# Kernel optimization log

Hardware: AMD Instinct MI355X
Metric: run time of the kernel (lower is better)

Reference implementation:

```python
import jax, jax.numpy as jnp
import numpy as np
from jax import lax

B, C, H, W = 16, 128, 128, 128
COUT, KH, KW, K, RED, TEMP = 128, 3, 3, 4, 4, 30.0
ATTN_CH = max(C // RED, 1)

def setup_inputs() -> dict:
    key = jax.random.key(0)
    ks = jax.random.split(key, 7)
    fan_out = COUT * KH * KW
    std = np.sqrt(2.0 / fan_out)  # kaiming_normal fan_out, relu
    return {
        "x": jax.random.normal(ks[0], (B, C, H, W), dtype=jnp.float32),
        "weight": jax.random.normal(ks[1], (K, COUT, C, KH, KW), dtype=jnp.float32) * std,
        "bias": jnp.zeros((K, COUT), dtype=jnp.float32),
        "aw1": jax.random.normal(ks[2], (ATTN_CH, C), dtype=jnp.float32) * (1.0 / np.sqrt(C)),
        "ab1": jnp.zeros((ATTN_CH,), dtype=jnp.float32),
        "aw2": jax.random.normal(ks[3], (K, ATTN_CH), dtype=jnp.float32) * (1.0 / np.sqrt(ATTN_CH)),
        "ab2": jnp.zeros((K,), dtype=jnp.float32),
    }

def reference(x, weight, bias, aw1, ab1, aw2, ab2):
    # Attention branch: global avg pool -> 1x1 conv -> relu -> 1x1 conv
    pooled = jnp.mean(x, axis=(2, 3))                       # (B, C)
    h = jax.nn.relu(pooled @ aw1.T + ab1)                   # (B, attn_ch)
    scores = h @ aw2.T + ab2                                # (B, K)
    attn = jax.nn.softmax(scores / TEMP, axis=1)            # (B, K)

    # Per-sample aggregated kernel and bias
    agg_w = jnp.einsum('bk,koipq->boipq', attn, weight)     # (B, Cout, Cin, kH, kW)
    agg_b = attn @ bias                                     # (B, Cout)

    # Per-sample conv2d (stride 1, padding 1, dilation 1, groups 1)
    def conv_one(xi, wi):
        return lax.conv_general_dilated(
            xi[None], wi,
            window_strides=(1, 1),
            padding=((1, 1), (1, 1)),
            dimension_numbers=('NCHW', 'OIHW', 'NCHW'),
        )[0]

    out = jax.vmap(conv_one)(x, agg_w)                      # (B, Cout, H, W)
    return out + agg_b[:, :, None, None]
```

## Files before the change

### kernel.cpp

```cpp
#include <hip/hip_runtime.h>

typedef float f32x4 __attribute__((ext_vector_type(4)));
typedef short bf16x8 __attribute__((ext_vector_type(8)));

__device__ __forceinline__ unsigned short f2bf(float f) {
  unsigned u = __builtin_bit_cast(unsigned, f);
  u = (u + 0x7FFFu + ((u >> 16) & 1u)) >> 16;
  return (unsigned short)u;
}

__device__ __forceinline__ void async16(const unsigned short* g, unsigned short* l) {
  __builtin_amdgcn_global_load_lds(
      (__attribute__((address_space(1))) void*)g,
      (__attribute__((address_space(3))) void*)l, 16, 0, 0);
}

#define XT_ROW 16640

__global__ __launch_bounds__(256) void k_transpose(const float* __restrict__ x,
                                                   unsigned short* __restrict__ xt,
                                                   float* __restrict__ rowsum) {
  __shared__ unsigned short tile[128][128];
  __shared__ float psum[128][8];
  const int y = blockIdx.x, b = blockIdx.y;
  const int t = threadIdx.x;
  const int colb = (t & 7) * 16;
  const int cp = t >> 3;
  const int swz = (t & 7) << 3;
  for (int ci = 0; ci < 4; ++ci) {
    const int c = ci * 32 + cp;
    const int c2 = c ^ swz;
    const float* src = x + (((size_t)(b * 128 + c) * 128 + y) * 128 + colb);
    float s = 0.f;
#pragma unroll
    for (int j = 0; j < 16; j += 4) {
      float4 v = *(const float4*)(src + j);
      s += v.x + v.y + v.z + v.w;
      tile[colb + j + 0][c2] = f2bf(v.x);
      tile[colb + j + 1][c2] = f2bf(v.y);
      tile[colb + j + 2][c2] = f2bf(v.z);
      tile[colb + j + 3][c2] = f2bf(v.w);
    }
    psum[c][t & 7] = s;
  }
  __syncthreads();
#pragma unroll
  for (int it = 0; it < 8; ++it) {
    const int slot = t + it * 256;
    const int col = slot >> 4;
    const int cg = (slot & 15) * 8;
    const int c2 = cg ^ (((col >> 4) & 7) << 3);
    uint4 vv = *(const uint4*)&tile[col][c2];
    *(uint4*)(xt + (((size_t)b * 130 + y + 1) * 130 + col + 1) * 128 + cg) = vv;
  }
  if (t < 128) {
    float r = 0.f;
#pragma unroll
    for (int j = 0; j < 8; ++j) r += psum[t][j];
    rowsum[((size_t)b * 128 + t) * 128 + y] = r;
  }
}

__global__ __launch_bounds__(256) void k_border(unsigned short* __restrict__ xt) {
  const int b = blockIdx.y;
  const int idx = blockIdx.x * 256 + threadIdx.x;
  if (idx >= 8256) return;
  int row, col, ck;
  if (idx < 4160) {
    row = (idx < 2080) ? 0 : 129;
    const int s = idx % 2080;
    col = s >> 4;
    ck = s & 15;
  } else {
    const int s = idx - 4160;
    row = (s >> 5) + 1;
    col = (s & 16) ? 129 : 0;
    ck = s & 15;
  }
  uint4 z = {0, 0, 0, 0};
  *(uint4*)(xt + ((size_t)b * 130 + row) * 130 * 128 + (size_t)col * 128 + ck * 8) = z;
}

__global__ __launch_bounds__(128) void k_attn(const float* __restrict__ rowsum,
                                              const float* __restrict__ aw1,
                                              const float* __restrict__ ab1,
                                              const float* __restrict__ aw2,
                                              const float* __restrict__ ab2,
                                              const float* __restrict__ bias,
                                              float* __restrict__ attn,
                                              float* __restrict__ aggb) {
  __shared__ float pooled[128];
  __shared__ float h[32];
  __shared__ float at[4];
  const int b = blockIdx.x, t = threadIdx.x;
  const float* rs = rowsum + (size_t)(b * 128 + t) * 128;
  float s = 0.f;
  for (int yy = 0; yy < 128; ++yy) s += rs[yy];
  pooled[t] = s * (1.f / 16384.f);
  __syncthreads();
  if (t < 32) {
    float hv = ab1[t];
    for (int c = 0; c < 128; ++c) hv += pooled[c] * aw1[t * 128 + c];
    h[t] = fmaxf(hv, 0.f);
  }
  __syncthreads();
  if (t < 4) {
    float sc = ab2[t];
    for (int a = 0; a < 32; ++a) sc += h[a] * aw2[t * 32 + a];
    at[t] = sc * (1.f / 30.f);
  }
  __syncthreads();
  if (t == 0) {
    float m = fmaxf(fmaxf(at[0], at[1]), fmaxf(at[2], at[3]));
    float e0 = __expf(at[0] - m), e1 = __expf(at[1] - m);
    float e2 = __expf(at[2] - m), e3 = __expf(at[3] - m);
    float inv = 1.f / (e0 + e1 + e2 + e3);
    at[0] = e0 * inv; at[1] = e1 * inv; at[2] = e2 * inv; at[3] = e3 * inv;
  }
  __syncthreads();
  if (t < 4) attn[b * 4 + t] = at[t];
  float ab = 0.f;
  for (int k = 0; k < 4; ++k) ab += at[k] * bias[k * 128 + t];
  aggb[b * 128 + t] = ab;
}

__global__ __launch_bounds__(256) void k_aggw(const float* __restrict__ weight,
                                              const float* __restrict__ attn,
                                              unsigned short* __restrict__ aggw) {
  const int fid = blockIdx.x * 256 + threadIdx.x;
  const int kk = fid & 63;
  const int o = (fid >> 6) & 127;
  const int rest = fid >> 13;
  const int s = rest % 18;
  const int b = rest / 18;
  const int c = ((s & 1) << 6) + kk;
  const int pq = s >> 1;
  const size_t src = (size_t)o * 1152 + (size_t)c * 9 + pq;
  float v = attn[b * 4 + 0] * weight[src]
          + attn[b * 4 + 1] * weight[src + 147456]
          + attn[b * 4 + 2] * weight[src + 2 * 147456]
          + attn[b * 4 + 3] * weight[src + 3 * 147456];
  aggw[fid] = f2bf(v);
}

__global__ __launch_bounds__(512, 2) void k_conv(const unsigned short* __restrict__ xt,
                                                 const unsigned short* __restrict__ aggw,
                                                 const float* __restrict__ aggb,
                                                 float* __restrict__ out) {
  __shared__ unsigned short lds[3][24576];
  const int id = blockIdx.x;
  const int swz = (id & 7) * 128 + (id >> 3);
  const int b = swz >> 6;
  const int y0 = (swz & 63) * 2;
  const int t = threadIdx.x;
  const int lane = t & 63, w = t >> 6;
  const int mw = w >> 2, nw = w & 3;
  const int l15 = lane & 15, lk = lane >> 4;
  const int rswz = (l15 & 7) * 8;

  const unsigned short* aS[2];
  int aD[2];
#pragma unroll
  for (int i = 0; i < 2; ++i) {
    const int ca = w * 128 + i * 64 + lane;
    const int n = ca >> 3, k8 = ca & 7;
    aS[i] = aggw + (size_t)b * 147456 + n * 64 + ((k8 ^ (n & 7)) * 8);
    aD[i] = w * 1024 + i * 512;
  }
  const unsigned short* bS[4];
  int bD[4];
#pragma unroll
  for (int i = 0; i < 4; ++i) {
    const int cb = w * 256 + i * 64 + lane;
    const int r = cb >> 10, n = (cb >> 3) & 127, k8 = cb & 7;
    bS[i] = xt + ((size_t)(b * 130 + y0 + r) * 130 + n) * 128 + ((k8 ^ (n & 7)) * 8);
    bD[i] = 8192 + w * 2048 + i * 512;
  }

#define STAGE(buf, s) {                                                        \
    const int tap_ = (s) >> 1, c0_ = ((s) & 1) << 6;                           \
    const int p_ = tap_ / 3, q_ = tap_ - 3 * p_;                               \
    _Pragma("unroll")                                                          \
    for (int i = 0; i < 2; ++i)                                                \
      async16(aS[i] + (s) * 8192, &lds[buf][0] + aD[i]);                       \
    _Pragma("unroll")                                                          \
    for (int i = 0; i < 4; ++i)                                                \
      async16(bS[i] + p_ * XT_ROW + q_ * 128 + c0_, &lds[buf][0] + bD[i]);     \
  }

  f32x4 acc[4][4] = {};
  STAGE(0, 0);
  STAGE(1, 1);

#pragma unroll
  for (int s = 0; s < 18; ++s) {
    const int cur = s % 3;
    if (s < 17) { asm volatile("s_waitcnt vmcnt(6)" ::: "memory"); }
    else       { asm volatile("s_waitcnt vmcnt(0)" ::: "memory"); }
    __builtin_amdgcn_sched_barrier(0);
    __builtin_amdgcn_s_barrier();
    __builtin_amdgcn_sched_barrier(0);
    if (s + 2 < 18) STAGE((s + 2) % 3, s + 2);
    __builtin_amdgcn_sched_barrier(0);

    const unsigned short* A0 = &lds[cur][0];
    const unsigned short* B0 = &lds[cur][8192];
#pragma unroll
    for (int kk = 0; kk < 2; ++kk) {
      bf16x8 af[4], bfr[4];
#pragma unroll
      for (int mi = 0; mi < 4; ++mi)
        af[mi] = *(const bf16x8*)(A0 + (mw * 64 + mi * 16 + l15) * 64
                                     + ((kk * 32 + lk * 8) ^ rswz));
#pragma unroll
      for (int ni = 0; ni < 4; ++ni)
        bfr[ni] = *(const bf16x8*)(B0 + (nw * 64 + ni * 16 + l15) * 64
                                      + ((kk * 32 + lk * 8) ^ rswz));
      __builtin_amdgcn_s_setprio(1);
#pragma unroll
      for (int mi = 0; mi < 4; ++mi)
#pragma unroll
        for (int ni = 0; ni < 4; ++ni)
          acc[mi][ni] = __builtin_amdgcn_mfma_f32_16x16x32_bf16(af[mi], bfr[ni], acc[mi][ni], 0, 0, 0);
      __builtin_amdgcn_s_setprio(0);
    }
  }
#undef STAGE

  const int r_ = nw >> 1;
  const int y = y0 + r_;
  const int colb = (nw & 1) * 64 + l15;
#pragma unroll
  for (int mi = 0; mi < 4; ++mi) {
    const int o = mw * 64 + mi * 16 + lk * 4;
#pragma unroll
    for (int rr = 0; rr < 4; ++rr) {
      const float bsv = aggb[b * 128 + o + rr];
      float* orow = out + ((size_t)(b * 128 + o + rr) * 128 + y) * 128 + colb;
      orow[0]  = acc[mi][0][rr] + bsv;
      orow[16] = acc[mi][1][rr] + bsv;
      orow[32] = acc[mi][2][rr] + bsv;
      orow[48] = acc[mi][3][rr] + bsv;
    }
  }
}

extern "C" void kernel_launch(void* const* d_in, const int* in_sizes, int n_in,
                              void* d_out, int out_size, void* d_ws, size_t ws_size,
                              hipStream_t stream) {
  const float* x      = (const float*)d_in[0];
  const float* weight = (const float*)d_in[1];
  const float* bias   = (const float*)d_in[2];
  const float* aw1    = (const float*)d_in[3];
  const float* ab1    = (const float*)d_in[4];
  const float* aw2    = (const float*)d_in[5];
  const float* ab2    = (const float*)d_in[6];
  float* out = (float*)d_out;

  char* ws = (char*)d_ws;
  unsigned short* xt   = (unsigned short*)ws;
  unsigned short* aggw = (unsigned short*)(ws + 69222400);
  float* rowsum        = (float*)(ws + 69222400 + 4718592);
  float* attn          = (float*)(ws + 69222400 + 4718592 + 1048576);
  float* aggb          = (float*)(ws + 69222400 + 4718592 + 1048576 + 256);

  hipLaunchKernelGGL(k_border, dim3(33, 16), dim3(256), 0, stream, xt);
  hipLaunchKernelGGL(k_transpose, dim3(128, 16), dim3(256), 0, stream, x, xt, rowsum);
  hipLaunchKernelGGL(k_attn, dim3(16), dim3(128), 0, stream,
                     rowsum, aw1, ab1, aw2, ab2, bias, attn, aggb);
  hipLaunchKernelGGL(k_aggw, dim3(9216), dim3(256), 0, stream, weight, attn, aggw);
  hipLaunchKernelGGL(k_conv, dim3(1024), dim3(512), 0, stream, xt, aggw, aggb, out);
}
```

Baseline: 158.3 us.

## Shrink conv tile to one output row with 32-channel K slices and 3 blocks/CU

The conv kernel now computes one output row (128 out channels x 128 pixels) per 256-thread block instead of two rows per 512-thread block. The K dimension is split into 36 stages of 32 channels instead of 18 stages of 64, so LDS use per block drops threefold and occupancy rises to 3 blocks per CU. The aggregated-weight layout and the LDS swizzle are changed to match the 32-wide chunks. The aim is more concurrent blocks to hide latency, at the cost of twice as many barriers per unit of work and less reuse of the weight tile across rows.

```diff
diff --git a/kernel.cpp b/kernel.cpp
--- a/kernel.cpp
+++ b/kernel.cpp
@@ -128,13 +128,13 @@
                                               const float* __restrict__ attn,
                                               unsigned short* __restrict__ aggw) {
   const int fid = blockIdx.x * 256 + threadIdx.x;
-  const int kk = fid & 63;
-  const int o = (fid >> 6) & 127;
-  const int rest = fid >> 13;
-  const int s = rest % 18;
-  const int b = rest / 18;
-  const int c = ((s & 1) << 6) + kk;
-  const int pq = s >> 1;
+  const int kk = fid & 31;
+  const int o = (fid >> 5) & 127;
+  const int rest = fid >> 12;
+  const int s = rest % 36;
+  const int b = rest / 36;
+  const int c = ((s & 3) << 5) + kk;
+  const int pq = s >> 2;
   const size_t src = (size_t)o * 1152 + (size_t)c * 9 + pq;
   float v = attn[b * 4 + 0] * weight[src]
           + attn[b * 4 + 1] * weight[src + 147456]
@@ -143,49 +143,41 @@
   aggw[fid] = f2bf(v);
 }
 
-__global__ __launch_bounds__(512, 2) void k_conv(const unsigned short* __restrict__ xt,
+__global__ __launch_bounds__(256, 3) void k_conv(const unsigned short* __restrict__ xt,
                                                  const unsigned short* __restrict__ aggw,
                                                  const float* __restrict__ aggb,
                                                  float* __restrict__ out) {
-  __shared__ unsigned short lds[3][24576];
+  __shared__ unsigned short lds[3][8192];
   const int id = blockIdx.x;
-  const int swz = (id & 7) * 128 + (id >> 3);
-  const int b = swz >> 6;
-  const int y0 = (swz & 63) * 2;
+  const int swz = (id & 7) * 256 + (id >> 3);
+  const int b = swz >> 7, y = swz & 127;
   const int t = threadIdx.x;
   const int lane = t & 63, w = t >> 6;
-  const int mw = w >> 2, nw = w & 3;
+  const int mw = w >> 1, nw = w & 1;
   const int l15 = lane & 15, lk = lane >> 4;
-  const int rswz = (l15 & 7) * 8;
+  const int rswz = (l15 & 3) * 8;
 
   const unsigned short* aS[2];
-  int aD[2];
+  const unsigned short* bS[2];
+  int dA[2], dB[2];
 #pragma unroll
   for (int i = 0; i < 2; ++i) {
-    const int ca = w * 128 + i * 64 + lane;
-    const int n = ca >> 3, k8 = ca & 7;
-    aS[i] = aggw + (size_t)b * 147456 + n * 64 + ((k8 ^ (n & 7)) * 8);
-    aD[i] = w * 1024 + i * 512;
-  }
-  const unsigned short* bS[4];
-  int bD[4];
-#pragma unroll
-  for (int i = 0; i < 4; ++i) {
-    const int cb = w * 256 + i * 64 + lane;
-    const int r = cb >> 10, n = (cb >> 3) & 127, k8 = cb & 7;
-    bS[i] = xt + ((size_t)(b * 130 + y0 + r) * 130 + n) * 128 + ((k8 ^ (n & 7)) * 8);
-    bD[i] = 8192 + w * 2048 + i * 512;
+    const int c = i * 256 + t;
+    const int n = c >> 2, k8 = c & 3;
+    const int sk = (k8 ^ (n & 3)) * 8;
+    aS[i] = aggw + (size_t)b * 147456 + n * 32 + sk;
+    bS[i] = xt + ((size_t)(b * 130 + y) * 130 + n) * 128 + sk;
+    dA[i] = i * 2048 + w * 512;
+    dB[i] = 4096 + i * 2048 + w * 512;
   }
 
 #define STAGE(buf, s) {                                                        \
-    const int tap_ = (s) >> 1, c0_ = ((s) & 1) << 6;                           \
+    const int tap_ = (s) >> 2, c0_ = ((s) & 3) << 5;                           \
     const int p_ = tap_ / 3, q_ = tap_ - 3 * p_;                               \
-    _Pragma("unroll")                                                          \
-    for (int i = 0; i < 2; ++i)                                                \
-      async16(aS[i] + (s) * 8192, &lds[buf][0] + aD[i]);                       \
-    _Pragma("unroll")                                                          \
-    for (int i = 0; i < 4; ++i)                                                \
-      async16(bS[i] + p_ * XT_ROW + q_ * 128 + c0_, &lds[buf][0] + bD[i]);     \
+    async16(aS[0] + (s) * 4096, &lds[buf][0] + dA[0]);                         \
+    async16(aS[1] + (s) * 4096, &lds[buf][0] + dA[1]);                         \
+    async16(bS[0] + p_ * XT_ROW + q_ * 128 + c0_, &lds[buf][0] + dB[0]);       \
+    async16(bS[1] + p_ * XT_ROW + q_ * 128 + c0_, &lds[buf][0] + dB[1]);       \
   }
 
   f32x4 acc[4][4] = {};
@@ -193,43 +185,40 @@
   STAGE(1, 1);
 
 #pragma unroll
-  for (int s = 0; s < 18; ++s) {
+  for (int s = 0; s < 36; ++s) {
     const int cur = s % 3;
-    if (s < 17) { asm volatile("s_waitcnt vmcnt(6)" ::: "memory"); }
-    else       { asm volatile("s_waitcnt vmcnt(0)" ::: "memory"); }
+    if (s < 35) { asm volatile("s_waitcnt vmcnt(4)" ::: "memory"); }
+    else        { asm volatile("s_waitcnt vmcnt(0)" ::: "memory"); }
     __builtin_amdgcn_sched_barrier(0);
     __builtin_amdgcn_s_barrier();
     __builtin_amdgcn_sched_barrier(0);
-    if (s + 2 < 18) STAGE((s + 2) % 3, s + 2);
+    if (s + 2 < 36) STAGE((s + 2) % 3, s + 2);
     __builtin_amdgcn_sched_barrier(0);
 
     const unsigned short* A0 = &lds[cur][0];
-    const unsigned short* B0 = &lds[cur][8192];
-#pragma unroll
-    for (int kk = 0; kk < 2; ++kk) {
-      bf16x8 af[4], bfr[4];
-#pragma unroll
-      for (int mi = 0; mi < 4; ++mi)
-        af[mi] = *(const bf16x8*)(A0 + (mw * 64 + mi * 16 + l15) * 64
-                                     + ((kk * 32 + lk * 8) ^ rswz));
+    const unsigned short* B0 = &lds[cur][4096];
+    bf16x8 af[4], bfr[4];
+#pragma unroll
+    for (int mi = 0; mi < 4; ++mi) {
+      const int row = mw * 64 + mi * 16 + l15;
+      af[mi] = *(const bf16x8*)(A0 + row * 32 + ((lk * 8) ^ rswz));
+    }
+#pragma unroll
+    for (int ni = 0; ni < 4; ++ni) {
+      const int row = nw * 64 + ni * 16 + l15;
+      bfr[ni] = *(const bf16x8*)(B0 + row * 32 + ((lk * 8) ^ rswz));
+    }
+    __builtin_amdgcn_s_setprio(1);
+#pragma unroll
+    for (int mi = 0; mi < 4; ++mi)
 #pragma unroll
       for (int ni = 0; ni < 4; ++ni)
-        bfr[ni] = *(const bf16x8*)(B0 + (nw * 64 + ni * 16 + l15) * 64
-                                      + ((kk * 32 + lk * 8) ^ rswz));
-      __builtin_amdgcn_s_setprio(1);
-#pragma unroll
-      for (int mi = 0; mi < 4; ++mi)
-#pragma unroll
-        for (int ni = 0; ni < 4; ++ni)
-          acc[mi][ni] = __builtin_amdgcn_mfma_f32_16x16x32_bf16(af[mi], bfr[ni], acc[mi][ni], 0, 0, 0);
-      __builtin_amdgcn_s_setprio(0);
-    }
+        acc[mi][ni] = __builtin_amdgcn_mfma_f32_16x16x32_bf16(af[mi], bfr[ni], acc[mi][ni], 0, 0, 0);
+    __builtin_amdgcn_s_setprio(0);
   }
 #undef STAGE
 
-  const int r_ = nw >> 1;
-  const int y = y0 + r_;
-  const int colb = (nw & 1) * 64 + l15;
+  const int colb = nw * 64 + l15;
 #pragma unroll
   for (int mi = 0; mi < 4; ++mi) {
     const int o = mw * 64 + mi * 16 + lk * 4;
@@ -269,5 +258,5 @@
   hipLaunchKernelGGL(k_attn, dim3(16), dim3(128), 0, stream,
                      rowsum, aw1, ab1, aw2, ab2, bias, attn, aggb);
   hipLaunchKernelGGL(k_aggw, dim3(9216), dim3(256), 0, stream, weight, attn, aggw);
-  hipLaunchKernelGGL(k_conv, dim3(1024), dim3(512), 0, stream, xt, aggw, aggb, out);
-}
+  hipLaunchKernelGGL(k_conv, dim3(2048), dim3(256), 0, stream, xt, aggw, aggb, out);
+}
```

Result: faster. 149.7 us (-5.4%).

## Interleave async global-to-LDS loads with MFMA phases in conv mainloop

Applied to the files above, without the earlier changes.

Restructures the conv K-loop into four compute phases, each preceded by a small batch of LDS fragment reads and a slice of the next-next stage's async global-to-LDS loads, separated by workgroup barriers. The goal is to spread memory issue across the MFMA work instead of issuing it all at the top of each stage, in a ping-pong style schedule. Launch bounds drop from 2 to 1 waves per SIMD hint, which permits more registers but may cut occupancy. The extra barriers per stage add synchronization overhead.

```diff
diff --git a/kernel.cpp b/kernel.cpp
--- a/kernel.cpp
+++ b/kernel.cpp
@@ -143,92 +143,139 @@
   aggw[fid] = f2bf(v);
 }
 
-__global__ __launch_bounds__(512, 2) void k_conv(const unsigned short* __restrict__ xt,
+__global__ __launch_bounds__(512, 1) void k_conv(const unsigned short* __restrict__ xt,
                                                  const unsigned short* __restrict__ aggw,
                                                  const float* __restrict__ aggb,
                                                  float* __restrict__ out) {
-  __shared__ unsigned short lds[3][24576];
+  __shared__ unsigned short lds[73728];
   const int id = blockIdx.x;
   const int swz = (id & 7) * 128 + (id >> 3);
   const int b = swz >> 6;
-  const int y0 = (swz & 63) * 2;
+  const int Y = (swz & 63) * 2;
   const int t = threadIdx.x;
   const int lane = t & 63, w = t >> 6;
   const int mw = w >> 2, nw = w & 3;
   const int l15 = lane & 15, lk = lane >> 4;
-  const int rswz = (l15 & 7) * 8;
+  const int e7 = l15 & 7;
+  const int sl0 = (lk ^ e7) * 8;
+  const int sl1 = ((4 ^ lk) ^ e7) * 8;
+  const int baseA0 = (mw * 64 + l15) * 64 + sl0;
+  const int baseA1 = (mw * 64 + l15) * 64 + sl1;
+  const int baseB0 = 8192 + (nw * 64 + l15) * 64 + sl0;
+  const int baseB1 = 8192 + (nw * 64 + l15) * 64 + sl1;
 
   const unsigned short* aS[2];
-  int aD[2];
 #pragma unroll
   for (int i = 0; i < 2; ++i) {
-    const int ca = w * 128 + i * 64 + lane;
-    const int n = ca >> 3, k8 = ca & 7;
-    aS[i] = aggw + (size_t)b * 147456 + n * 64 + ((k8 ^ (n & 7)) * 8);
-    aD[i] = w * 1024 + i * 512;
+    const int c = i * 512 + t, o = c >> 3, k8 = c & 7;
+    aS[i] = aggw + (size_t)b * 147456 + o * 64 + ((k8 ^ (o & 7)) * 8);
   }
   const unsigned short* bS[4];
-  int bD[4];
 #pragma unroll
   for (int i = 0; i < 4; ++i) {
-    const int cb = w * 256 + i * 64 + lane;
-    const int r = cb >> 10, n = (cb >> 3) & 127, k8 = cb & 7;
-    bS[i] = xt + ((size_t)(b * 130 + y0 + r) * 130 + n) * 128 + ((k8 ^ (n & 7)) * 8);
-    bD[i] = 8192 + w * 2048 + i * 512;
-  }
-
-#define STAGE(buf, s) {                                                        \
-    const int tap_ = (s) >> 1, c0_ = ((s) & 1) << 6;                           \
-    const int p_ = tap_ / 3, q_ = tap_ - 3 * p_;                               \
-    _Pragma("unroll")                                                          \
-    for (int i = 0; i < 2; ++i)                                                \
-      async16(aS[i] + (s) * 8192, &lds[buf][0] + aD[i]);                       \
-    _Pragma("unroll")                                                          \
-    for (int i = 0; i < 4; ++i)                                                \
-      async16(bS[i] + p_ * XT_ROW + q_ * 128 + c0_, &lds[buf][0] + bD[i]);     \
-  }
+    const int c = i * 512 + t, n = c >> 3, k8 = c & 7;
+    const int r = n >> 7, col = n & 127;
+    bS[i] = xt + ((size_t)(b * 130 + Y + r) * 130 + col) * 128 + ((k8 ^ (n & 7)) * 8);
+  }
+
+#define STA(jw, s2, i) async16(aS[i] + (s2) * 8192,                            \
+                               &lds[(jw) * 24576 + ((i) * 512 + w * 64) * 8])
+#define STB(jw, i, p2, q2, c02) async16(bS[i] + (p2) * XT_ROW + (q2) * 128 + (c02), \
+                               &lds[(jw) * 24576 + 8192 + ((i) * 512 + w * 64) * 8])
+
+  STA(0, 0, 0); STA(0, 0, 1);
+  STB(0, 0, 0, 0, 0); STB(0, 1, 0, 0, 0); STB(0, 2, 0, 0, 0); STB(0, 3, 0, 0, 0);
+  STA(1, 1, 0); STA(1, 1, 1);
+  STB(1, 0, 0, 0, 64); STB(1, 1, 0, 0, 64); STB(1, 2, 0, 0, 64); STB(1, 3, 0, 0, 64);
 
   f32x4 acc[4][4] = {};
-  STAGE(0, 0);
-  STAGE(1, 1);
 
 #pragma unroll
   for (int s = 0; s < 18; ++s) {
-    const int cur = s % 3;
+    const int jb = (s % 3) * 24576;
+    const int s2 = s + 2, jw = s2 % 3;
+    const int tap2 = s2 >> 1;
+    const int p2 = tap2 / 3, q2 = tap2 - 3 * p2, c02 = (s2 & 1) << 6;
+    const bool st = (s2 < 18);
+
     if (s < 17) { asm volatile("s_waitcnt vmcnt(6)" ::: "memory"); }
-    else       { asm volatile("s_waitcnt vmcnt(0)" ::: "memory"); }
+    else        { asm volatile("s_waitcnt vmcnt(0)" ::: "memory"); }
     __builtin_amdgcn_sched_barrier(0);
     __builtin_amdgcn_s_barrier();
     __builtin_amdgcn_sched_barrier(0);
-    if (s + 2 < 18) STAGE((s + 2) % 3, s + 2);
-    __builtin_amdgcn_sched_barrier(0);
-
-    const unsigned short* A0 = &lds[cur][0];
-    const unsigned short* B0 = &lds[cur][8192];
-#pragma unroll
-    for (int kk = 0; kk < 2; ++kk) {
-      bf16x8 af[4], bfr[4];
-#pragma unroll
-      for (int mi = 0; mi < 4; ++mi)
-        af[mi] = *(const bf16x8*)(A0 + (mw * 64 + mi * 16 + l15) * 64
-                                     + ((kk * 32 + lk * 8) ^ rswz));
-#pragma unroll
-      for (int ni = 0; ni < 4; ++ni)
-        bfr[ni] = *(const bf16x8*)(B0 + (nw * 64 + ni * 16 + l15) * 64
-                                      + ((kk * 32 + lk * 8) ^ rswz));
-      __builtin_amdgcn_s_setprio(1);
-#pragma unroll
-      for (int mi = 0; mi < 4; ++mi)
-#pragma unroll
-        for (int ni = 0; ni < 4; ++ni)
-          acc[mi][ni] = __builtin_amdgcn_mfma_f32_16x16x32_bf16(af[mi], bfr[ni], acc[mi][ni], 0, 0, 0);
-      __builtin_amdgcn_s_setprio(0);
-    }
-  }
-#undef STAGE
-
-  const int r_ = nw >> 1;
-  const int y = y0 + r_;
+
+    bf16x8 a0, a1, a2, a3, b0, b1, b2, b3;
+    b0 = *(const bf16x8*)(&lds[jb + baseB0 + 0 * 1024]);
+    b1 = *(const bf16x8*)(&lds[jb + baseB0 + 1 * 1024]);
+    b2 = *(const bf16x8*)(&lds[jb + baseB0 + 2 * 1024]);
+    b3 = *(const bf16x8*)(&lds[jb + baseB0 + 3 * 1024]);
+    a0 = *(const bf16x8*)(&lds[jb + baseA0 + 0 * 1024]);
+    a1 = *(const bf16x8*)(&lds[jb + baseA0 + 1 * 1024]);
+    if (st) { STA(jw, s2, 0); STA(jw, s2, 1); }
+    __builtin_amdgcn_s_barrier();
+    __builtin_amdgcn_s_setprio(1);
+    acc[0][0] = __builtin_amdgcn_mfma_f32_16x16x32_bf16(a0, b0, acc[0][0], 0, 0, 0);
+    acc[0][1] = __builtin_amdgcn_mfma_f32_16x16x32_bf16(a0, b1, acc[0][1], 0, 0, 0);
+    acc[0][2] = __builtin_amdgcn_mfma_f32_16x16x32_bf16(a0, b2, acc[0][2], 0, 0, 0);
+    acc[0][3] = __builtin_amdgcn_mfma_f32_16x16x32_bf16(a0, b3, acc[0][3], 0, 0, 0);
+    acc[1][0] = __builtin_amdgcn_mfma_f32_16x16x32_bf16(a1, b0, acc[1][0], 0, 0, 0);
+    acc[1][1] = __builtin_amdgcn_mfma_f32_16x16x32_bf16(a1, b1, acc[1][1], 0, 0, 0);
+    acc[1][2] = __builtin_amdgcn_mfma_f32_16x16x32_bf16(a1, b2, acc[1][2], 0, 0, 0);
+    acc[1][3] = __builtin_amdgcn_mfma_f32_16x16x32_bf16(a1, b3, acc[1][3], 0, 0, 0);
+    __builtin_amdgcn_s_setprio(0);
+    __builtin_amdgcn_s_barrier();
+    a2 = *(const bf16x8*)(&lds[jb + baseA0 + 2 * 1024]);
+    a3 = *(const bf16x8*)(&lds[jb + baseA0 + 3 * 1024]);
+    if (st) { STB(jw, 0, p2, q2, c02); STB(jw, 1, p2, q2, c02); }
+    __builtin_amdgcn_s_barrier();
+    __builtin_amdgcn_s_setprio(1);
+    acc[2][0] = __builtin_amdgcn_mfma_f32_16x16x32_bf16(a2, b0, acc[2][0], 0, 0, 0);
+    acc[2][1] = __builtin_amdgcn_mfma_f32_16x16x32_bf16(a2, b1, acc[2][1], 0, 0, 0);
+    acc[2][2] = __builtin_amdgcn_mfma_f32_16x16x32_bf16(a2, b2, acc[2][2], 0, 0, 0);
+    acc[2][3] = __builtin_amdgcn_mfma_f32_16x16x32_bf16(a2, b3, acc[2][3], 0, 0, 0);
+    acc[3][0] = __builtin_amdgcn_mfma_f32_16x16x32_bf16(a3, b0, acc[3][0], 0, 0, 0);
+    acc[3][1] = __builtin_amdgcn_mfma_f32_16x16x32_bf16(a3, b1, acc[3][1], 0, 0, 0);
+    acc[3][2] = __builtin_amdgcn_mfma_f32_16x16x32_bf16(a3, b2, acc[3][2], 0, 0, 0);
+    acc[3][3] = __builtin_amdgcn_mfma_f32_16x16x32_bf16(a3, b3, acc[3][3], 0, 0, 0);
+    __builtin_amdgcn_s_setprio(0);
+    __builtin_amdgcn_s_barrier();
+    b0 = *(const bf16x8*)(&lds[jb + baseB1 + 0 * 1024]);
+    b1 = *(const bf16x8*)(&lds[jb + baseB1 + 1 * 1024]);
+    b2 = *(const bf16x8*)(&lds[jb + baseB1 + 2 * 1024]);
+    b3 = *(const bf16x8*)(&lds[jb + baseB1 + 3 * 1024]);
+    a0 = *(const bf16x8*)(&lds[jb + baseA1 + 0 * 1024]);
+    a1 = *(const bf16x8*)(&lds[jb + baseA1 + 1 * 1024]);
+    if (st) { STB(jw, 2, p2, q2, c02); STB(jw, 3, p2, q2, c02); }
+    __builtin_amdgcn_s_barrier();
+    __builtin_amdgcn_s_setprio(1);
+    acc[0][0] = __builtin_amdgcn_mfma_f32_16x16x32_bf16(a0, b0, acc[0][0], 0, 0, 0);
+    acc[0][1] = __builtin_amdgcn_mfma_f32_16x16x32_bf16(a0, b1, acc[0][1], 0, 0, 0);
+    acc[0][2] = __builtin_amdgcn_mfma_f32_16x16x32_bf16(a0, b2, acc[0][2], 0, 0, 0);
+    acc[0][3] = __builtin_amdgcn_mfma_f32_16x16x32_bf16(a0, b3, acc[0][3], 0, 0, 0);
+    acc[1][0] = __builtin_amdgcn_mfma_f32_16x16x32_bf16(a1, b0, acc[1][0], 0, 0, 0);
+    acc[1][1] = __builtin_amdgcn_mfma_f32_16x16x32_bf16(a1, b1, acc[1][1], 0, 0, 0);
+    acc[1][2] = __builtin_amdgcn_mfma_f32_16x16x32_bf16(a1, b2, acc[1][2], 0, 0, 0);
+    acc[1][3] = __builtin_amdgcn_mfma_f32_16x16x32_bf16(a1, b3, acc[1][3], 0, 0, 0);
+    __builtin_amdgcn_s_setprio(0);
+    __builtin_amdgcn_s_barrier();
+    a2 = *(const bf16x8*)(&lds[jb + baseA1 + 2 * 1024]);
+    a3 = *(const bf16x8*)(&lds[jb + baseA1 + 3 * 1024]);
+    __builtin_amdgcn_s_barrier();
+    __builtin_amdgcn_s_setprio(1);
+    acc[2][0] = __builtin_amdgcn_mfma_f32_16x16x32_bf16(a2, b0, acc[2][0], 0, 0, 0);
+    acc[2][1] = __builtin_amdgcn_mfma_f32_16x16x32_bf16(a2, b1, acc[2][1], 0, 0, 0);
+    acc[2][2] = __builtin_amdgcn_mfma_f32_16x16x32_bf16(a2, b2, acc[2][2], 0, 0, 0);
+    acc[2][3] = __builtin_amdgcn_mfma_f32_16x16x32_bf16(a2, b3, acc[2][3], 0, 0, 0);
+    acc[3][0] = __builtin_amdgcn_mfma_f32_16x16x32_bf16(a3, b0, acc[3][0], 0, 0, 0);
+    acc[3][1] = __builtin_amdgcn_mfma_f32_16x16x32_bf16(a3, b1, acc[3][1], 0, 0, 0);
+    acc[3][2] = __builtin_amdgcn_mfma_f32_16x16x32_bf16(a3, b2, acc[3][2], 0, 0, 0);
+    acc[3][3] = __builtin_amdgcn_mfma_f32_16x16x32_bf16(a3, b3, acc[3][3], 0, 0, 0);
+    __builtin_amdgcn_s_setprio(0);
+  }
+#undef STA
+#undef STB
+
+  const int y = Y + (nw >> 1);
   const int colb = (nw & 1) * 64 + l15;
 #pragma unroll
   for (int mi = 0; mi < 4; ++mi) {
```

New measurement: 157.8 us. Within noise of the previous version (-0.3%).
